# Kernel optimization log

Hardware: AMD Instinct MI355X
Metric: run time of the kernel (lower is better)

The kernel has to match this reference:

```python
import jax, jax.numpy as jnp
import numpy as np
from functools import partial

H = 2048   # image height
W = 2048   # image width
FC_IN = 1024
FC_OUT = 10


def setup_inputs() -> dict:
    key = jax.random.key(0)
    ks = jax.random.split(key, 7)
    x = jax.random.normal(ks[0], (1, H, W), dtype=jnp.float32)
    # Conv2d(1,1,1): scalar weight + bias
    w_in = jax.random.normal(ks[1], (1, 1, 1, 1), dtype=jnp.float32)
    b_in = jax.random.normal(ks[2], (1,), dtype=jnp.float32) * 0.1
    # Conv1d(1,1,2,padding=1): 2-tap kernel + bias
    w_state = jax.random.normal(ks[3], (1, 1, 2), dtype=jnp.float32) * 0.5
    b_state = jax.random.normal(ks[4], (1,), dtype=jnp.float32) * 0.1
    # Linear(1024, 10)
    fc_w = jax.random.normal(ks[5], (FC_OUT, FC_IN), dtype=jnp.float32) * (1.0 / np.sqrt(FC_IN))
    fc_b = jax.random.normal(ks[6], (FC_OUT,), dtype=jnp.float32) * 0.1
    return {"x": x, "w_in": w_in, "b_in": b_in, "w_state": w_state,
            "b_state": b_state, "fc_w": fc_w, "fc_b": fc_b}


def reference(x, w_in, b_in, w_state, b_state, fc_w, fc_b):
    img = x[0]                      # [H, W]
    h_dim, w_dim = img.shape
    w_skew = w_dim + h_dim - 1      # skewed image width

    # --- skew: row r shifted right by r, zero-filled elsewhere ---
    rows = jnp.arange(h_dim)[:, None]          # [H,1]
    cols = jnp.arange(w_dim)[None, :] + rows   # [H,W] destination columns
    skewed = jnp.zeros((h_dim, w_skew), dtype=img.dtype).at[rows, cols].set(img)

    # --- 1x1 input convolution: scalar affine ---
    input_matrix = skewed * w_in[0, 0, 0, 0] + b_in[0]   # [H, Wskew]

    k0 = w_state[0, 0, 0]
    k1 = w_state[0, 0, 1]
    bs = b_state[0]

    # --- sequential column scan: h_c = tanh(k0*shift(h) + k1*h + bs + inp_c) ---
    def step(h, inp_col):
        shifted = jnp.concatenate([jnp.zeros((1,), h.dtype), h[:-1]])
        a = jnp.tanh(k0 * shifted + k1 * h + bs + inp_col)
        return a, a

    h0 = jnp.zeros((h_dim,), dtype=img.dtype)
    _, acts = jax.lax.scan(step, h0, input_matrix.T)     # acts: [Wskew, H]

    # --- unskew: unskewed[r, c] = acts[r + c, r] ---
    c_idx = jnp.arange(w_dim)[None, :]                   # [1, W]
    unskewed = acts[rows + c_idx, rows]                  # [H, W]

    flat = unskewed.reshape(-1, FC_IN)                   # [H*W/1024, 1024]
    return flat @ fc_w.T + fc_b                          # [H*W/1024, 10]
```

## Files before the change

kernel.cpp:

```cpp
#include <hip/hip_runtime.h>

#define HH 2048
#define WW 2048
#define WSK 4095
#define WSKP 4096
#define BLKS 8
#define NW  4
#define NT  (NW * 64)
#define KCH 32
#define NCH (WSKP / KCH)
#define FC_IN 1024
#define FC_OUT 10
#define NFLAT ((HH * WW) / FC_IN)

#define MRING 2048

__device__ __forceinline__ float tanh_pre(float xs) {
  float e = __builtin_amdgcn_exp2f(xs);
  float r = __builtin_amdgcn_rcpf(e + 1.0f);
  return __builtin_fmaf(-2.0f, r, 1.0f);
}

__device__ __forceinline__ float wave_shr1(float src, float old) {
  int r = __builtin_amdgcn_update_dpp(
      __builtin_bit_cast(int, old), __builtin_bit_cast(int, src),
      0x138 , 0xF, 0xF, false);
  return __builtin_bit_cast(float, r);
}

__global__ __launch_bounds__(256) void skew_kernel(
    const float* __restrict__ img, const float* __restrict__ w_in,
    const float* __restrict__ b_in, const float* __restrict__ b_state,
    float* __restrict__ inp) {
  const float S = 2.88539008177792681472f;
  const float ws = w_in[0] * S;
  const float Cs = (b_in[0] + b_state[0]) * S;
  int gid = blockIdx.x * 256 + threadIdx.x;
  int r = gid & (HH - 1);
  int c = gid >> 11;
  int idx = c - r;
  float v = Cs;
  if ((unsigned)idx < (unsigned)WW) v = fmaf(ws, img[(size_t)r * WW + idx], Cs);
  inp[gid] = v;
}

__global__ __launch_bounds__(NT) void scan_kernel(
    const float* __restrict__ w_state, const float* __restrict__ inp,
    float* __restrict__ acts, unsigned long long* __restrict__ mbox) {
  const int t = threadIdx.x;
  const int wv = t >> 6;
  const int lane = t & 63;
  const int blk = blockIdx.x;
  const int r = blk * NT + t;

  const float S = 2.88539008177792681472f;
  const float k0s = w_state[0] * S;
  const float k1s = w_state[1] * S;

  __shared__ float ring[2][NW][KCH];

  float h = 0.0f;
  const float* colp_in = inp + r;
  float* colp_out = acts + r;

  float pf[KCH];
  #pragma unroll
  for (int d = 0; d < KCH; ++d) pf[d] = colp_in[(size_t)d * HH];

  unsigned long long praw = 0;
  if (wv == 0 && blk > 0 && lane < KCH) {
    unsigned long long* mb_up = mbox + (size_t)(blk - 1) * MRING;
    int cl = lane - 1;
    praw = __hip_atomic_load(&mb_up[cl & (MRING - 1)], __ATOMIC_RELAXED,
                             __HIP_MEMORY_SCOPE_AGENT);
  }

  for (int e = 0; e < NCH + NW - 1; ++e) {
    const int ch = e - wv;
    if (0 <= ch && ch < NCH) {
      const int c0 = ch * KCH;

      float bvec;
      if (wv == 0) {
        bvec = 0.0f;
        if (blk > 0) {
          unsigned long long* mb_up = mbox + (size_t)(blk - 1) * MRING;
          const int cl = c0 + lane - 1;
          const bool need = (lane < KCH) && (cl >= 0);
          const unsigned want = (unsigned)(cl + 1);
          unsigned long long raw = praw;
          while (!__all((!need) || ((unsigned)(raw >> 32) == want))) {
            __builtin_amdgcn_s_sleep(1);
            if (need)
              raw = __hip_atomic_load(&mb_up[cl & (MRING - 1)],
                                      __ATOMIC_RELAXED,
                                      __HIP_MEMORY_SCOPE_AGENT);
          }
          if (need) bvec = __builtin_bit_cast(float, (unsigned)raw);
          if (lane < KCH)
            praw = __hip_atomic_load(&mb_up[(cl + KCH) & (MRING - 1)],
                                     __ATOMIC_RELAXED,
                                     __HIP_MEMORY_SCOPE_AGENT);
        }
      } else {
        bvec = ring[(e & 1) ^ 1][wv - 1][lane & (KCH - 1)];
      }
      if (lane == 63 && wv != NW - 1) ring[e & 1][wv][0] = h;

      if (wv == NW - 1 && blk + 1 < BLKS) {
        const int cmax = c0 + KCH - 1;
        if (cmax >= MRING) {
          unsigned long long* mb_dn = mbox + (size_t)(blk + 1) * MRING;
          const int cref = cmax - (MRING - 128);
          const unsigned wantt = (unsigned)(cref + 1);
          if (lane == 63) {
            while ((unsigned)(__hip_atomic_load(&mb_dn[cref & (MRING - 1)],
                       __ATOMIC_RELAXED, __HIP_MEMORY_SCOPE_AGENT) >> 32)
                   != wantt)
              __builtin_amdgcn_s_sleep(8);
          }
        }
      }

      const int cb = (ch + 1 < NCH ? ch + 1 : ch) * KCH;
      unsigned long long* mb_my = mbox + (size_t)blk * MRING;

      #pragma unroll
      for (int cc = 0; cc < KCH; ++cc) {
        float cur = pf[cc];
        pf[cc] = colp_in[(size_t)(cb + cc) * HH];

        float pv = __builtin_bit_cast(float,
            __builtin_amdgcn_readlane(__builtin_bit_cast(int, bvec), cc));
        float prev = wave_shr1(h, pv);

        h = tanh_pre(fmaf(k0s, prev, fmaf(k1s, h, cur)));

        if (lane == 63) {
          if (wv != NW - 1) {
            if (cc + 1 < KCH) ring[e & 1][wv][cc + 1] = h;
          } else {
            unsigned long long pack =
                ((unsigned long long)(unsigned)(c0 + cc + 1) << 32) |
                (unsigned long long)__builtin_bit_cast(unsigned, h);
            __hip_atomic_store(&mb_my[(c0 + cc) & (MRING - 1)], pack,
                               __ATOMIC_RELAXED, __HIP_MEMORY_SCOPE_AGENT);
          }
        }
        colp_out[(size_t)(c0 + cc) * HH] = h;
      }
    }
    asm volatile("s_waitcnt lgkmcnt(0)\n\ts_barrier" ::: "memory");
  }
}

#define FCR 16
#define FCCH 256
#define FCT 256

__global__ __launch_bounds__(FCT) void fc_kernel(
    const float* __restrict__ acts, const float* __restrict__ fc_w,
    const float* __restrict__ fc_b, float* __restrict__ out) {
  __shared__ float fcw[FC_OUT * FC_IN];
  __shared__ float tile[FCCH][FCR + 1];

  const int tid = threadIdx.x;
  const int bb = blockIdx.x;
  const int r0 = bb * FCR;

  for (int i = tid; i < FC_OUT * FC_IN; i += FCT) fcw[i] = fc_w[i];

  const int il = tid >> 3;
  const int cs = tid & 7;
  const int rloc = il >> 1;
  const int koff = (r0 + rloc) + ((il & 1) << 10);

  const int lrr = tid & 15;
  const int lco = tid >> 4;

  float acc[FC_OUT];
  #pragma unroll
  for (int j = 0; j < FC_OUT; ++j) acc[j] = 0.0f;

  __syncthreads();

  const int cend = r0 + FCR - 1 + 2047;
  for (int cb = r0; cb <= cend; cb += FCCH) {
    #pragma unroll
    for (int s = 0; s < FCCH / 16; ++s) {
      int cc = s * 16 + lco;
      int col = cb + cc;
      int colc = col < WSK ? col : (WSK - 1);
      tile[cc][lrr] = acts[(size_t)colc * HH + r0 + lrr];
    }
    __syncthreads();

    #pragma unroll 4
    for (int tt = 0; tt < FCCH / 8; ++tt) {
      int cc = tt * 8 + cs;
      int k = cb + cc - koff;
      if (0 <= k && k < FC_IN) {
        float v = tile[cc][rloc];
        #pragma unroll
        for (int j = 0; j < FC_OUT; ++j)
          acc[j] = fmaf(v, fcw[j * FC_IN + k], acc[j]);
      }
    }
    __syncthreads();
  }

  #pragma unroll
  for (int j = 0; j < FC_OUT; ++j) {
    acc[j] += __shfl_down(acc[j], 4, 8);
    acc[j] += __shfl_down(acc[j], 2, 8);
    acc[j] += __shfl_down(acc[j], 1, 8);
  }
  if (cs == 0) {
    const int i = bb * 32 + il;
    #pragma unroll
    for (int j = 0; j < FC_OUT; ++j) out[i * FC_OUT + j] = acc[j] + fc_b[j];
  }
}

extern "C" void kernel_launch(void* const* d_in, const int* in_sizes, int n_in,
                              void* d_out, int out_size, void* d_ws, size_t ws_size,
                              hipStream_t stream) {
  const float* x       = (const float*)d_in[0];
  const float* w_in    = (const float*)d_in[1];
  const float* b_in    = (const float*)d_in[2];
  const float* w_state = (const float*)d_in[3];
  const float* b_state = (const float*)d_in[4];
  const float* fc_w    = (const float*)d_in[5];
  const float* fc_b    = (const float*)d_in[6];
  float* out = (float*)d_out;
  float* buf = (float*)d_ws;

  unsigned long long* mbox = (unsigned long long*)d_out;

  skew_kernel<<<(WSKP * HH) / 256, 256, 0, stream>>>(x, w_in, b_in, b_state, buf);
  scan_kernel<<<BLKS, NT, 0, stream>>>(w_state, buf, buf, mbox);
  fc_kernel<<<HH / FCR, FCT, 0, stream>>>(buf, fc_w, fc_b, out);
}
```

Before: 643.4 us.

## Double scan chunk width and move cross-block mailbox wait to end of chunk

Raises the column chunk size of the wavefront scan from 32 to 64, halving the number of chunk iterations and the barriers between them. Wave 0 now waits for the upstream block's boundary values for the next chunk right after finishing the current chunk, instead of at the start of each chunk. The mailbox loads use acquire ordering in place of relaxed. In exchange the prefetch register array doubles, which raises register pressure. Larger chunks also lengthen the pipeline fill between the waves and between blocks.

```diff
diff --git a/kernel.cpp b/kernel.cpp
--- a/kernel.cpp
+++ b/kernel.cpp
@@ -7,7 +7,7 @@
 #define BLKS 8
 #define NW  4
 #define NT  (NW * 64)
-#define KCH 32
+#define KCH 64
 #define NCH (WSKP / KCH)
 #define FC_IN 1024
 #define FC_OUT 10
@@ -68,11 +68,20 @@
   for (int d = 0; d < KCH; ++d) pf[d] = colp_in[(size_t)d * HH];
 
   unsigned long long praw = 0;
-  if (wv == 0 && blk > 0 && lane < KCH) {
+  if (wv == 0 && blk > 0) {
     unsigned long long* mb_up = mbox + (size_t)(blk - 1) * MRING;
-    int cl = lane - 1;
-    praw = __hip_atomic_load(&mb_up[cl & (MRING - 1)], __ATOMIC_RELAXED,
-                             __HIP_MEMORY_SCOPE_AGENT);
+    const int cl = lane - 1;
+    const bool need = (cl >= 0);
+    const unsigned want = (unsigned)(cl + 1);
+    if (need)
+      praw = __hip_atomic_load(&mb_up[cl & (MRING - 1)], __ATOMIC_ACQUIRE,
+                               __HIP_MEMORY_SCOPE_AGENT);
+    while (!__all((!need) || ((unsigned)(praw >> 32) == want))) {
+      __builtin_amdgcn_s_sleep(1);
+      if (need)
+        praw = __hip_atomic_load(&mb_up[cl & (MRING - 1)], __ATOMIC_ACQUIRE,
+                                 __HIP_MEMORY_SCOPE_AGENT);
+    }
   }
 
   for (int e = 0; e < NCH + NW - 1; ++e) {
@@ -84,26 +93,11 @@
       if (wv == 0) {
         bvec = 0.0f;
         if (blk > 0) {
-          unsigned long long* mb_up = mbox + (size_t)(blk - 1) * MRING;
           const int cl = c0 + lane - 1;
-          const bool need = (lane < KCH) && (cl >= 0);
-          const unsigned want = (unsigned)(cl + 1);
-          unsigned long long raw = praw;
-          while (!__all((!need) || ((unsigned)(raw >> 32) == want))) {
-            __builtin_amdgcn_s_sleep(1);
-            if (need)
-              raw = __hip_atomic_load(&mb_up[cl & (MRING - 1)],
-                                      __ATOMIC_RELAXED,
-                                      __HIP_MEMORY_SCOPE_AGENT);
-          }
-          if (need) bvec = __builtin_bit_cast(float, (unsigned)raw);
-          if (lane < KCH)
-            praw = __hip_atomic_load(&mb_up[(cl + KCH) & (MRING - 1)],
-                                     __ATOMIC_RELAXED,
-                                     __HIP_MEMORY_SCOPE_AGENT);
+          if (cl >= 0) bvec = __builtin_bit_cast(float, (unsigned)praw);
         }
       } else {
-        bvec = ring[(e & 1) ^ 1][wv - 1][lane & (KCH - 1)];
+        bvec = ring[(e & 1) ^ 1][wv - 1][lane];
       }
       if (lane == 63 && wv != NW - 1) ring[e & 1][wv][0] = h;
 
@@ -149,6 +143,20 @@
         }
         colp_out[(size_t)(c0 + cc) * HH] = h;
       }
+
+      if (wv == 0 && blk > 0 && ch + 1 < NCH) {
+        unsigned long long* mb_up = mbox + (size_t)(blk - 1) * MRING;
+        const int cl2 = (ch + 1) * KCH + lane - 1;
+        const unsigned want = (unsigned)(cl2 + 1);
+        praw = __hip_atomic_load(&mb_up[cl2 & (MRING - 1)], __ATOMIC_ACQUIRE,
+                                 __HIP_MEMORY_SCOPE_AGENT);
+        while (!__all((unsigned)(praw >> 32) == want)) {
+          __builtin_amdgcn_s_sleep(1);
+          praw = __hip_atomic_load(&mb_up[cl2 & (MRING - 1)],
+                                   __ATOMIC_ACQUIRE,
+                                   __HIP_MEMORY_SCOPE_AGENT);
+        }
+      }
     }
     asm volatile("s_waitcnt lgkmcnt(0)\n\ts_barrier" ::: "memory");
   }
```

Result: slower. 679.1 us (+5.6%).
